# Performance work log

Measured on AMD Instinct MI355X. Metric: run time of the kernel, lower is better.

The kernel has to match this reference:

```python
import jax, jax.numpy as jnp
import numpy as np

N_NODES = 50000


def gcn_conv(x, W, b, row, col, n):
    # PyG GCNConv with default improved=False, add_self_loops=True:
    # h = X W; deg_i = 1 + sum_{e: col==i} 1; out_i = sum_e dinv[row]*dinv[col]*h[row] + h_i/deg_i + b
    h = x @ W  # [N, out]
    ones = jnp.ones(row.shape[0], dtype=x.dtype)
    deg = jax.ops.segment_sum(ones, col, num_segments=n) + 1.0  # self-loop included
    dinv = jax.lax.rsqrt(deg)
    coef = (dinv[row] * dinv[col])[:, None]  # [E,1]
    msg = h[row] * coef  # edge-wise gather (memory bound)
    agg = jax.ops.segment_sum(msg, col, num_segments=n)
    agg = agg + h * (1.0 / deg)[:, None]  # self-loop contribution
    return agg + b


def setup_inputs() -> dict:
    key = jax.random.key(0)
    ks = jax.random.split(key, 7)
    nfeats, nhids, proj = 128, 128, 4
    h2 = nhids + proj  # 132
    x = jax.random.normal(ks[0], (N_NODES, nfeats), dtype=jnp.float32)
    edge_index = jax.random.randint(ks[1], (2, 800000), 0, N_NODES, dtype=jnp.int64)
    s = 1.0 / np.sqrt(nfeats)
    W_proj = jax.random.normal(ks[2], (nfeats, proj), dtype=jnp.float32) * s
    W1 = jax.random.normal(ks[3], (nfeats, nhids), dtype=jnp.float32) * s
    b1 = jax.random.normal(ks[4], (nhids,), dtype=jnp.float32) * 0.01
    s2 = 1.0 / np.sqrt(h2)
    W2 = jax.random.normal(ks[5], (h2, h2), dtype=jnp.float32) * s2
    b2 = jax.random.normal(ks[6], (h2,), dtype=jnp.float32) * 0.01
    return {"edge_index": edge_index, "x": x, "W_proj": W_proj,
            "W1": W1, "b1": b1, "W2": W2, "b2": b2}


def reference(edge_index, x, W_proj, W1, b1, W2, b2):
    row, col = edge_index[0], edge_index[1]
    n = x.shape[0]
    x_proj = x @ W_proj  # [N, proj]
    h = jax.nn.relu(gcn_conv(x, W1, b1, row, col, n))
    # dropout in eval mode (identity)
    h = jnp.concatenate([h, x_proj], axis=1)  # concat skip -> [N, nhids+proj]
    h = gcn_conv(h, W2, b2, row, col, n)
    return jnp.concatenate([h, x_proj], axis=1)  # [N, nhids+2*proj]
```

## Files before the change

kernel.cpp:

```cpp
#include <hip/hip_runtime.h>

#define NN   50000
#define MPAD 50048

#define NB    196
#define SLOTS 48
#define PT_T  512
#define PT_TILE 4096
#define CAP   5888
#define BT    256

typedef __attribute__((ext_vector_type(8))) short bf16x8;
typedef __attribute__((ext_vector_type(4))) float f32x4;
typedef unsigned int  u32;
typedef unsigned short u16;

__device__ __forceinline__ u16 f2bf(float f) {
    u32 u = __float_as_uint(f);
    return (u16)((u + 0x7fffu + ((u >> 16) & 1u)) >> 16);
}
__device__ __forceinline__ float bflo(u32 u) { return __uint_as_float(u << 16); }
__device__ __forceinline__ float bfhi(u32 u) { return __uint_as_float(u & 0xffff0000u); }
__device__ __forceinline__ u32 pack2(float x, float y) {
    return (u32)f2bf(x) | ((u32)f2bf(y) << 16);
}


__global__ void k_zinit(int* __restrict__ gcnt) {
    int i = threadIdx.x;
    if (i < NB) gcnt[i] = 0;
}

__global__ __launch_bounds__(PT_T) void k_bhist(const int* __restrict__ ecol, int E,
                                                int* __restrict__ gcnt) {
    __shared__ int lh[NB];
    int tid = threadIdx.x;
    for (int i = tid; i < NB; i += PT_T) lh[i] = 0;
    __syncthreads();
    int e0 = blockIdx.x * PT_TILE;
#pragma unroll
    for (int j = 0; j < PT_TILE / PT_T; ++j) {
        int e = e0 + j * PT_T + tid;
        if (e < E) atomicAdd(&lh[ecol[e] >> 8], 1);
    }
    __syncthreads();
    for (int i = tid; i < NB; i += PT_T)
        if (lh[i]) atomicAdd(&gcnt[i], lh[i]);
}

__global__ void k_bscan(const int* __restrict__ gcnt, int* __restrict__ gbase,
                        int* __restrict__ gcursor, int* __restrict__ starts, int E) {
    __shared__ int a[256];
    int tid = threadIdx.x;
    int v = (tid < NB) ? gcnt[tid] : 0;
    a[tid] = v;
    __syncthreads();
    for (int off = 1; off < 256; off <<= 1) {
        int add = (tid >= off) ? a[tid - off] : 0;
        __syncthreads();
        a[tid] += add;
        __syncthreads();
    }
    int exc = a[tid] - v;
    if (tid < NB) { gbase[tid] = exc; gcursor[tid] = exc; }
    if (tid == NB - 1) gbase[NB] = a[tid];
    if (tid == 0) starts[NN] = E;
}

__global__ __launch_bounds__(PT_T) void k_part(const int* __restrict__ erow,
                                               const int* __restrict__ ecol, int E,
                                               int* __restrict__ gcursor,
                                               u32* __restrict__ recs) {
    __shared__ int lcnt[NB];
    __shared__ int bbase[NB];
    __shared__ u32 rbuf[NB * SLOTS];
    int tid = threadIdx.x;
    for (int i = tid; i < NB; i += PT_T) lcnt[i] = 0;
    __syncthreads();
    int e0 = blockIdx.x * PT_TILE;
#pragma unroll
    for (int j = 0; j < PT_TILE / PT_T; ++j) {
        int e = e0 + j * PT_T + tid;
        if (e < E) {
            int c = ecol[e];
            u32 rec = ((u32)(c & 255) << 24) | (u32)erow[e];
            int b = c >> 8;
            int pos = atomicAdd(&lcnt[b], 1);
            if (pos < SLOTS) rbuf[b * SLOTS + pos] = rec;
            else {
                int g = atomicAdd(&gcursor[b], 1);
                if (g >= 0 && g < E) recs[g] = rec;
            }
        }
    }
    __syncthreads();
    if (tid < NB) {
        int n = lcnt[tid]; if (n > SLOTS) n = SLOTS;
        bbase[tid] = n ? atomicAdd(&gcursor[tid], n) : 0;
    }
    __syncthreads();
    int wave = tid >> 6, lane = tid & 63;
    for (int b = wave; b < NB; b += PT_T / 64) {
        int n = lcnt[b]; if (n > SLOTS) n = SLOTS;
        if (lane < n) {
            int g = bbase[b] + lane;
            if (g >= 0 && g < E) recs[g] = rbuf[b * SLOTS + lane];
        }
    }
}

__global__ __launch_bounds__(BT) void k_build(const u32* __restrict__ recs,
                                              const int* __restrict__ gbase,
                                              int* __restrict__ starts,
                                              float* __restrict__ dinv,
                                              u32* __restrict__ ec) {
    __shared__ u32 rbuf[CAP];
    __shared__ u32 obuf[CAP];
    __shared__ int ncnt[256];
    __shared__ int a[256];
    __shared__ int ncur[256];
    int tid = threadIdx.x, b = blockIdx.x;
    int lo = gbase[b], hi = gbase[b + 1];
    int cnt = hi - lo;
    bool stage = (cnt > 0) && (cnt <= CAP);
    if (stage) for (int i = tid; i < cnt; i += BT) rbuf[i] = recs[lo + i];
    ncnt[tid] = 0;
    __syncthreads();
    for (int i = tid; i < cnt; i += BT) {
        u32 rec = stage ? rbuf[i] : recs[lo + i];
        atomicAdd(&ncnt[rec >> 24], 1);
    }
    __syncthreads();
    a[tid] = ncnt[tid];
    __syncthreads();
    for (int off = 1; off < 256; off <<= 1) {
        int add = (tid >= off) ? a[tid - off] : 0;
        __syncthreads();
        a[tid] += add;
        __syncthreads();
    }
    int excl = a[tid] - ncnt[tid];
    ncur[tid] = excl;
    {
        int node = (b << 8) + tid;
        if (node < NN) {
            starts[node] = lo + excl;
            float d = (float)ncnt[tid] + 1.0f;
            dinv[node] = rsqrtf(d);
        }
    }
    __syncthreads();
    for (int i = tid; i < cnt; i += BT) {
        u32 rec = stage ? rbuf[i] : recs[lo + i];
        int nl = rec >> 24;
        int pos = atomicAdd(&ncur[nl], 1);
        u32 r = rec & 0xFFFFFFu;
        if (stage) { if (pos >= 0 && pos < CAP) obuf[pos] = r; }
        else if (pos >= 0 && lo + pos < hi) ec[lo + pos] = r;
    }
    __syncthreads();
    if (stage) for (int i = tid; i < cnt; i += BT) ec[lo + i] = obuf[i];
}


__global__ void k_prep_w1(const float* __restrict__ W1, const float* __restrict__ Wp,
                          u16* __restrict__ Wt) {
    int i = blockIdx.x * blockDim.x + threadIdx.x;
    if (i >= 144 * 128) return;
    int n = i >> 7, k = i & 127;
    float v = 0.f;
    if (n < 128) v = W1[k * 128 + n];
    else if (n < 132) v = Wp[k * 4 + (n - 128)];
    Wt[i] = f2bf(v);
}

__global__ void k_prep_w2(const float* __restrict__ W2, u16* __restrict__ Wt) {
    int i = blockIdx.x * blockDim.x + threadIdx.x;
    if (i >= 144 * 160) return;
    int n = i / 160, k = i - n * 160;
    float v = (n < 132 && k < 132) ? W2[k * 132 + n] : 0.f;
    Wt[i] = f2bf(v);
}

template<int K, bool CONVF32, bool SCALE_EXT>
__global__ __launch_bounds__(256) void k_gemm_mfma(const void* __restrict__ Ain,
                                                   const u16* __restrict__ Bt,
                                                   const float* __restrict__ rs,
                                                   u16* __restrict__ Cmain,
                                                   u16* __restrict__ Cext) {
    int lane = threadIdx.x & 63;
    int wv = threadIdx.x >> 6;
    int rbase = blockIdx.x * 64 + wv * 16;
    int lr = lane & 15;
    int kk = (lane >> 4) * 8;
    int arow = rbase + lr;
    if (CONVF32 && arow >= NN) arow = NN - 1;

    const u16* bp = Bt + (size_t)lr * K + kk;

    f32x4 acc[9] = {};
#pragma unroll
    for (int ks = 0; ks < K / 32; ++ks) {
        bf16x8 af;
        if (CONVF32) {
            const float* ap = (const float*)Ain + (size_t)arow * K + kk + ks * 32;
            float4 f0 = *(const float4*)ap;
            float4 f1 = *(const float4*)(ap + 4);
            union { uint4 u; bf16x8 v; } cv;
            cv.u.x = pack2(f0.x, f0.y); cv.u.y = pack2(f0.z, f0.w);
            cv.u.z = pack2(f1.x, f1.y); cv.u.w = pack2(f1.z, f1.w);
            af = cv.v;
        } else {
            af = *(const bf16x8*)((const u16*)Ain + (size_t)arow * K + kk + ks * 32);
        }
#pragma unroll
        for (int t = 0; t < 9; ++t) {
            bf16x8 bf = *(const bf16x8*)(bp + (size_t)(t * 16) * K + ks * 32);
            acc[t] = __builtin_amdgcn_mfma_f32_16x16x32_bf16(bf, af, acc[t], 0, 0, 0);
        }
    }

    int n0 = (lane >> 4) * 4;
    int crow = rbase + lr;
    int srow = crow < NN ? crow : NN - 1;
    float s = rs[srow];
    u16* cm = Cmain + (size_t)crow * 128;
#pragma unroll
    for (int t = 0; t < 8; ++t) {
        ushort4 w;
        w.x = f2bf(acc[t][0] * s); w.y = f2bf(acc[t][1] * s);
        w.z = f2bf(acc[t][2] * s); w.w = f2bf(acc[t][3] * s);
        *(ushort4*)(cm + 16 * t + n0) = w;
    }
    if (n0 == 0) {
        float se = SCALE_EXT ? s : 1.0f;
        ushort4 w;
        w.x = f2bf(acc[8][0] * se); w.y = f2bf(acc[8][1] * se);
        w.z = f2bf(acc[8][2] * se); w.w = f2bf(acc[8][3] * se);
        *(ushort4*)(Cext + (size_t)crow * 4) = w;
    }
}


__global__ void k_agg1(const u16* __restrict__ Hm, const u16* __restrict__ Xp,
                       const int* __restrict__ starts, const u32* __restrict__ ec,
                       const float* __restrict__ dinv,
                       const float* __restrict__ b1, u16* __restrict__ outp) {
    int node = blockIdx.x * (blockDim.x >> 6) + (threadIdx.x >> 6);
    int lane = threadIdx.x & 63;
    if (node >= NN) return;
    int s = starts[node], e = starts[node + 1];

    u32 us = *(const u32*)(Hm + ((size_t)node << 7) + 2 * lane);
    float ax = bflo(us), ay = bfhi(us);
    int i = s;
    for (; i + 8 <= e; i += 8) {
        uint4 qa = *(const uint4*)(ec + i);
        uint4 qb = *(const uint4*)(ec + i + 4);
        u32 u0 = *(const u32*)(Hm + ((size_t)qa.x << 7) + 2 * lane);
        u32 u1 = *(const u32*)(Hm + ((size_t)qa.y << 7) + 2 * lane);
        u32 u2 = *(const u32*)(Hm + ((size_t)qa.z << 7) + 2 * lane);
        u32 u3 = *(const u32*)(Hm + ((size_t)qa.w << 7) + 2 * lane);
        u32 u4 = *(const u32*)(Hm + ((size_t)qb.x << 7) + 2 * lane);
        u32 u5 = *(const u32*)(Hm + ((size_t)qb.y << 7) + 2 * lane);
        u32 u6 = *(const u32*)(Hm + ((size_t)qb.z << 7) + 2 * lane);
        u32 u7 = *(const u32*)(Hm + ((size_t)qb.w << 7) + 2 * lane);
        ax += bflo(u0); ay += bfhi(u0); ax += bflo(u1); ay += bfhi(u1);
        ax += bflo(u2); ay += bfhi(u2); ax += bflo(u3); ay += bfhi(u3);
        ax += bflo(u4); ay += bfhi(u4); ax += bflo(u5); ay += bfhi(u5);
        ax += bflo(u6); ay += bfhi(u6); ax += bflo(u7); ay += bfhi(u7);
    }
    for (; i + 4 <= e; i += 4) {
        uint4 q = *(const uint4*)(ec + i);
        u32 u0 = *(const u32*)(Hm + ((size_t)q.x << 7) + 2 * lane);
        u32 u1 = *(const u32*)(Hm + ((size_t)q.y << 7) + 2 * lane);
        u32 u2 = *(const u32*)(Hm + ((size_t)q.z << 7) + 2 * lane);
        u32 u3 = *(const u32*)(Hm + ((size_t)q.w << 7) + 2 * lane);
        ax += bflo(u0); ay += bfhi(u0); ax += bflo(u1); ay += bfhi(u1);
        ax += bflo(u2); ay += bfhi(u2); ax += bflo(u3); ay += bfhi(u3);
    }
    for (; i < e; ++i) {
        u32 q = ec[i];
        u32 u = *(const u32*)(Hm + ((size_t)q << 7) + 2 * lane);
        ax += bflo(u); ay += bfhi(u);
    }

    float dc = dinv[node];
    float2 bv = *(const float2*)(b1 + 2 * lane);
    float vx = fmaxf(fmaf(dc, ax, bv.x), 0.f);
    float vy = fmaxf(fmaf(dc, ay, bv.y), 0.f);

    u32* orow = (u32*)(outp + (size_t)node * 160);
    orow[lane] = pack2(vx, vy);
    if (lane < 2) orow[64 + lane] = *(const u32*)(Xp + (size_t)node * 4 + 2 * lane);
    else if (lane < 16) orow[64 + lane] = 0;
}

__global__ void k_agg2(const u16* __restrict__ Hm, const u16* __restrict__ He,
                       const u16* __restrict__ Xp1,
                       const int* __restrict__ starts, const u32* __restrict__ ec,
                       const float* __restrict__ dinv,
                       const float* __restrict__ b2, float* __restrict__ outp) {
    int node = blockIdx.x * (blockDim.x >> 6) + (threadIdx.x >> 6);
    int lane = threadIdx.x & 63;
    if (node >= NN) return;
    int s = starts[node], e = starts[node + 1];

    u32 us = *(const u32*)(Hm + ((size_t)node << 7) + 2 * lane);
    float ax = bflo(us), ay = bfhi(us);
    float cx = 0.f, cy = 0.f;
    if (lane < 2) {
        u32 us2 = *(const u32*)(He + ((size_t)node << 2) + 2 * lane);
        cx = bflo(us2); cy = bfhi(us2);
    }
    int i = s;
    for (; i + 8 <= e; i += 8) {
        uint4 qa = *(const uint4*)(ec + i);
        uint4 qb = *(const uint4*)(ec + i + 4);
        u32 u0 = *(const u32*)(Hm + ((size_t)qa.x << 7) + 2 * lane);
        u32 u1 = *(const u32*)(Hm + ((size_t)qa.y << 7) + 2 * lane);
        u32 u2 = *(const u32*)(Hm + ((size_t)qa.z << 7) + 2 * lane);
        u32 u3 = *(const u32*)(Hm + ((size_t)qa.w << 7) + 2 * lane);
        u32 u4 = *(const u32*)(Hm + ((size_t)qb.x << 7) + 2 * lane);
        u32 u5 = *(const u32*)(Hm + ((size_t)qb.y << 7) + 2 * lane);
        u32 u6 = *(const u32*)(Hm + ((size_t)qb.z << 7) + 2 * lane);
        u32 u7 = *(const u32*)(Hm + ((size_t)qb.w << 7) + 2 * lane);
        ax += bflo(u0); ay += bfhi(u0); ax += bflo(u1); ay += bfhi(u1);
        ax += bflo(u2); ay += bfhi(u2); ax += bflo(u3); ay += bfhi(u3);
        ax += bflo(u4); ay += bfhi(u4); ax += bflo(u5); ay += bfhi(u5);
        ax += bflo(u6); ay += bfhi(u6); ax += bflo(u7); ay += bfhi(u7);
        if (lane < 2) {
            u32 e0 = *(const u32*)(He + ((size_t)qa.x << 2) + 2 * lane);
            u32 e1 = *(const u32*)(He + ((size_t)qa.y << 2) + 2 * lane);
            u32 e2 = *(const u32*)(He + ((size_t)qa.z << 2) + 2 * lane);
            u32 e3 = *(const u32*)(He + ((size_t)qa.w << 2) + 2 * lane);
            u32 e4 = *(const u32*)(He + ((size_t)qb.x << 2) + 2 * lane);
            u32 e5 = *(const u32*)(He + ((size_t)qb.y << 2) + 2 * lane);
            u32 e6 = *(const u32*)(He + ((size_t)qb.z << 2) + 2 * lane);
            u32 e7 = *(const u32*)(He + ((size_t)qb.w << 2) + 2 * lane);
            cx += bflo(e0); cy += bfhi(e0); cx += bflo(e1); cy += bfhi(e1);
            cx += bflo(e2); cy += bfhi(e2); cx += bflo(e3); cy += bfhi(e3);
            cx += bflo(e4); cy += bfhi(e4); cx += bflo(e5); cy += bfhi(e5);
            cx += bflo(e6); cy += bfhi(e6); cx += bflo(e7); cy += bfhi(e7);
        }
    }
    for (; i < e; ++i) {
        u32 q = ec[i];
        u32 u = *(const u32*)(Hm + ((size_t)q << 7) + 2 * lane);
        ax += bflo(u); ay += bfhi(u);
        if (lane < 2) {
            u32 e0 = *(const u32*)(He + ((size_t)q << 2) + 2 * lane);
            cx += bflo(e0); cy += bfhi(e0);
        }
    }

    float dc = dinv[node];
    float2 bv = *(const float2*)(b2 + 2 * lane);
    float vx = fmaf(dc, ax, bv.x);
    float vy = fmaf(dc, ay, bv.y);
    float* orow = outp + (size_t)node * 136;
    *(float2*)(orow + 2 * lane) = make_float2(vx, vy);

    if (lane < 2) {
        float2 bb = *(const float2*)(b2 + 128 + 2 * lane);
        float wx = fmaf(dc, cx, bb.x);
        float wy = fmaf(dc, cy, bb.y);
        *(float2*)(orow + 128 + 2 * lane) = make_float2(wx, wy);
        u32 up = *(const u32*)(Xp1 + ((size_t)node << 2) + 2 * lane);
        *(float2*)(orow + 132 + 2 * lane) = make_float2(bflo(up), bfhi(up));
    }
}

extern "C" void kernel_launch(void* const* d_in, const int* in_sizes, int n_in,
                              void* d_out, int out_size, void* d_ws, size_t ws_size,
                              hipStream_t stream) {
    const int*   ei = (const int*)d_in[0];
    const float* x  = (const float*)d_in[1];
    const float* Wp = (const float*)d_in[2];
    const float* W1 = (const float*)d_in[3];
    const float* b1 = (const float*)d_in[4];
    const float* W2 = (const float*)d_in[5];
    const float* b2 = (const float*)d_in[6];
    float* out = (float*)d_out;

    const int E = in_sizes[0] / 2;
    const int* erow = ei;
    const int* ecol = ei + E;

    char* p = (char*)d_ws;
    u16* H1main = (u16*)p; p += (size_t)MPAD * 128 * 2;
    u16* Hcat   = (u16*)p; p += (size_t)MPAD * 160 * 2;
    u16* Xp1    = (u16*)p; p += (size_t)MPAD * 4 * 2;
    u16* H2ext  = (u16*)p; p += (size_t)MPAD * 4 * 2;
    u16* W1t    = (u16*)p; p += 144 * 128 * 2;
    u16* W2t    = (u16*)p; p += 144 * 160 * 2;
    u32* recs   = (u32*)p; p += (size_t)E * 4;
    u32* ec     = (u32*)p; p += (size_t)E * 4;
    float* dinv   = (float*)p; p += NN * 4;
    int* starts = (int*)p; p += (size_t)(NN + 1) * 4;
    int* gcnt   = (int*)p; p += NB * 4;
    int* gbase  = (int*)p; p += (NB + 1) * 4;
    int* gcursor= (int*)p; p += NB * 4;

    u16* H2main = H1main;

    const int T = 256;
    const int pblocks = (E + PT_TILE - 1) / PT_TILE;

    k_prep_w1<<<(144 * 128 + T - 1) / T, T, 0, stream>>>(W1, Wp, W1t);
    k_prep_w2<<<(144 * 160 + T - 1) / T, T, 0, stream>>>(W2, W2t);

    k_zinit<<<1, 256, 0, stream>>>(gcnt);
    k_bhist<<<pblocks, PT_T, 0, stream>>>(ecol, E, gcnt);
    k_bscan<<<1, 256, 0, stream>>>(gcnt, gbase, gcursor, starts, E);
    k_part<<<pblocks, PT_T, 0, stream>>>(erow, ecol, E, gcursor, recs);
    k_build<<<NB, BT, 0, stream>>>(recs, gbase, starts, dinv, ec);

    const int gblocks = MPAD / 64;
    const int ablocks = (NN + 3) / 4;

    k_gemm_mfma<128, true, false><<<gblocks, T, 0, stream>>>(x, W1t, dinv, H1main, Xp1);
    k_agg1<<<ablocks, T, 0, stream>>>(H1main, Xp1, starts, ec, dinv, b1, Hcat);

    k_gemm_mfma<160, false, true><<<gblocks, T, 0, stream>>>(Hcat, W2t, dinv, H2main, H2ext);
    k_agg2<<<ablocks, T, 0, stream>>>(H2main, H2ext, Xp1, starts, ec, dinv, b2, out);
}
```

Before: 173.7 us.

## Split each wave into four 16-lane edge groups with 16-byte gathers

```diff
diff --git a/kernel.cpp b/kernel.cpp
--- a/kernel.cpp
+++ b/kernel.cpp
@@ -2,6 +2,7 @@
 
 #define NN   50000
 #define MPAD 50048
+#define ZR   NN
 
 #define NB    196
 #define SLOTS 48
@@ -222,8 +223,7 @@
 
     int n0 = (lane >> 4) * 4;
     int crow = rbase + lr;
-    int srow = crow < NN ? crow : NN - 1;
-    float s = rs[srow];
+    float s = (crow < NN) ? rs[crow] : 0.0f;
     u16* cm = Cmain + (size_t)crow * 128;
 #pragma unroll
     for (int t = 0; t < 8; ++t) {
@@ -233,7 +233,7 @@
         *(ushort4*)(cm + 16 * t + n0) = w;
     }
     if (n0 == 0) {
-        float se = SCALE_EXT ? s : 1.0f;
+        float se = SCALE_EXT ? s : ((crow < NN) ? 1.0f : 0.0f);
         ushort4 w;
         w.x = f2bf(acc[8][0] * se); w.y = f2bf(acc[8][1] * se);
         w.z = f2bf(acc[8][2] * se); w.w = f2bf(acc[8][3] * se);
@@ -242,61 +242,85 @@
 }
 
 
-__global__ void k_agg1(const u16* __restrict__ Hm, const u16* __restrict__ Xp,
+__global__ __launch_bounds__(256) void k_agg1(const u16* __restrict__ Hm,
+                       const u16* __restrict__ Xp,
                        const int* __restrict__ starts, const u32* __restrict__ ec,
                        const float* __restrict__ dinv,
                        const float* __restrict__ b1, u16* __restrict__ outp) {
     int node = blockIdx.x * (blockDim.x >> 6) + (threadIdx.x >> 6);
     int lane = threadIdx.x & 63;
-    if (node >= NN) return;
+    if (node >= MPAD) return;
+    int c16 = lane & 15;
+    u32* orow = (u32*)(outp + (size_t)node * 160);
+    if (node >= NN) {
+        if (lane < 16) {
+            *(uint4*)(orow + c16 * 4) = make_uint4(0, 0, 0, 0);
+            orow[64 + lane] = 0;
+        }
+        return;
+    }
+    int q = lane >> 4;
     int s = starts[node], e = starts[node + 1];
 
-    u32 us = *(const u32*)(Hm + ((size_t)node << 7) + 2 * lane);
-    float ax = bflo(us), ay = bfhi(us);
-    int i = s;
-    for (; i + 8 <= e; i += 8) {
-        uint4 qa = *(const uint4*)(ec + i);
-        uint4 qb = *(const uint4*)(ec + i + 4);
-        u32 u0 = *(const u32*)(Hm + ((size_t)qa.x << 7) + 2 * lane);
-        u32 u1 = *(const u32*)(Hm + ((size_t)qa.y << 7) + 2 * lane);
-        u32 u2 = *(const u32*)(Hm + ((size_t)qa.z << 7) + 2 * lane);
-        u32 u3 = *(const u32*)(Hm + ((size_t)qa.w << 7) + 2 * lane);
-        u32 u4 = *(const u32*)(Hm + ((size_t)qb.x << 7) + 2 * lane);
-        u32 u5 = *(const u32*)(Hm + ((size_t)qb.y << 7) + 2 * lane);
-        u32 u6 = *(const u32*)(Hm + ((size_t)qb.z << 7) + 2 * lane);
-        u32 u7 = *(const u32*)(Hm + ((size_t)qb.w << 7) + 2 * lane);
-        ax += bflo(u0); ay += bfhi(u0); ax += bflo(u1); ay += bfhi(u1);
-        ax += bflo(u2); ay += bfhi(u2); ax += bflo(u3); ay += bfhi(u3);
-        ax += bflo(u4); ay += bfhi(u4); ax += bflo(u5); ay += bfhi(u5);
-        ax += bflo(u6); ay += bfhi(u6); ax += bflo(u7); ay += bfhi(u7);
-    }
-    for (; i + 4 <= e; i += 4) {
-        uint4 q = *(const uint4*)(ec + i);
-        u32 u0 = *(const u32*)(Hm + ((size_t)q.x << 7) + 2 * lane);
-        u32 u1 = *(const u32*)(Hm + ((size_t)q.y << 7) + 2 * lane);
-        u32 u2 = *(const u32*)(Hm + ((size_t)q.z << 7) + 2 * lane);
-        u32 u3 = *(const u32*)(Hm + ((size_t)q.w << 7) + 2 * lane);
-        ax += bflo(u0); ay += bfhi(u0); ax += bflo(u1); ay += bfhi(u1);
-        ax += bflo(u2); ay += bfhi(u2); ax += bflo(u3); ay += bfhi(u3);
-    }
-    for (; i < e; ++i) {
-        u32 q = ec[i];
-        u32 u = *(const u32*)(Hm + ((size_t)q << 7) + 2 * lane);
-        ax += bflo(u); ay += bfhi(u);
-    }
+    float a0=0,a1=0,a2=0,a3=0,a4=0,a5=0,a6=0,a7=0;
+    if (lane < 16) {
+        uint4 v = *(const uint4*)(Hm + ((size_t)node << 7) + c16 * 8);
+        a0 = bflo(v.x); a1 = bfhi(v.x); a2 = bflo(v.y); a3 = bfhi(v.y);
+        a4 = bflo(v.z); a5 = bfhi(v.z); a6 = bflo(v.w); a7 = bfhi(v.w);
+    }
+
+    for (int g0 = s; g0 < e; g0 += 16) {
+        u32 row[4];
+#pragma unroll
+        for (int grp = 0; grp < 4; ++grp) {
+            int idx = g0 + grp * 4 + q;
+            int ii = idx < e ? idx : e - 1;
+            u32 r = ec[ii];
+            row[grp] = (idx < e) ? r : (u32)ZR;
+        }
+        uint4 v[4];
+#pragma unroll
+        for (int grp = 0; grp < 4; ++grp)
+            v[grp] = *(const uint4*)(Hm + ((size_t)row[grp] << 7) + c16 * 8);
+#pragma unroll
+        for (int grp = 0; grp < 4; ++grp) {
+            a0 += bflo(v[grp].x); a1 += bfhi(v[grp].x);
+            a2 += bflo(v[grp].y); a3 += bfhi(v[grp].y);
+            a4 += bflo(v[grp].z); a5 += bfhi(v[grp].z);
+            a6 += bflo(v[grp].w); a7 += bfhi(v[grp].w);
+        }
+    }
+
+    a0 += __shfl_xor(a0, 16); a1 += __shfl_xor(a1, 16);
+    a2 += __shfl_xor(a2, 16); a3 += __shfl_xor(a3, 16);
+    a4 += __shfl_xor(a4, 16); a5 += __shfl_xor(a5, 16);
+    a6 += __shfl_xor(a6, 16); a7 += __shfl_xor(a7, 16);
+    a0 += __shfl_xor(a0, 32); a1 += __shfl_xor(a1, 32);
+    a2 += __shfl_xor(a2, 32); a3 += __shfl_xor(a3, 32);
+    a4 += __shfl_xor(a4, 32); a5 += __shfl_xor(a5, 32);
+    a6 += __shfl_xor(a6, 32); a7 += __shfl_xor(a7, 32);
 
     float dc = dinv[node];
-    float2 bv = *(const float2*)(b1 + 2 * lane);
-    float vx = fmaxf(fmaf(dc, ax, bv.x), 0.f);
-    float vy = fmaxf(fmaf(dc, ay, bv.y), 0.f);
-
-    u32* orow = (u32*)(outp + (size_t)node * 160);
-    orow[lane] = pack2(vx, vy);
-    if (lane < 2) orow[64 + lane] = *(const u32*)(Xp + (size_t)node * 4 + 2 * lane);
-    else if (lane < 16) orow[64 + lane] = 0;
-}
-
-__global__ void k_agg2(const u16* __restrict__ Hm, const u16* __restrict__ He,
+    float4 bA = *(const float4*)(b1 + c16 * 8);
+    float4 bB = *(const float4*)(b1 + c16 * 8 + 4);
+    float v0 = fmaxf(fmaf(dc, a0, bA.x), 0.f);
+    float v1 = fmaxf(fmaf(dc, a1, bA.y), 0.f);
+    float v2 = fmaxf(fmaf(dc, a2, bA.z), 0.f);
+    float v3 = fmaxf(fmaf(dc, a3, bA.w), 0.f);
+    float v4 = fmaxf(fmaf(dc, a4, bB.x), 0.f);
+    float v5 = fmaxf(fmaf(dc, a5, bB.y), 0.f);
+    float v6 = fmaxf(fmaf(dc, a6, bB.z), 0.f);
+    float v7 = fmaxf(fmaf(dc, a7, bB.w), 0.f);
+
+    if (lane < 16) {
+        uint4 w = make_uint4(pack2(v0, v1), pack2(v2, v3), pack2(v4, v5), pack2(v6, v7));
+        *(uint4*)(orow + c16 * 4) = w;
+        orow[64 + lane] = (lane < 2) ? *(const u32*)(Xp + ((size_t)node << 2) + 2 * lane) : 0u;
+    }
+}
+
+__global__ __launch_bounds__(256) void k_agg2(const u16* __restrict__ Hm,
+                       const u16* __restrict__ He,
                        const u16* __restrict__ Xp1,
                        const int* __restrict__ starts, const u32* __restrict__ ec,
                        const float* __restrict__ dinv,
@@ -304,68 +328,78 @@
     int node = blockIdx.x * (blockDim.x >> 6) + (threadIdx.x >> 6);
     int lane = threadIdx.x & 63;
     if (node >= NN) return;
+    int c16 = lane & 15;
+    int q = lane >> 4;
     int s = starts[node], e = starts[node + 1];
 
-    u32 us = *(const u32*)(Hm + ((size_t)node << 7) + 2 * lane);
-    float ax = bflo(us), ay = bfhi(us);
+    float a0=0,a1=0,a2=0,a3=0,a4=0,a5=0,a6=0,a7=0;
     float cx = 0.f, cy = 0.f;
+    if (lane < 16) {
+        uint4 v = *(const uint4*)(Hm + ((size_t)node << 7) + c16 * 8);
+        a0 = bflo(v.x); a1 = bfhi(v.x); a2 = bflo(v.y); a3 = bfhi(v.y);
+        a4 = bflo(v.z); a5 = bfhi(v.z); a6 = bflo(v.w); a7 = bfhi(v.w);
+    }
     if (lane < 2) {
-        u32 us2 = *(const u32*)(He + ((size_t)node << 2) + 2 * lane);
-        cx = bflo(us2); cy = bfhi(us2);
-    }
-    int i = s;
-    for (; i + 8 <= e; i += 8) {
-        uint4 qa = *(const uint4*)(ec + i);
-        uint4 qb = *(const uint4*)(ec + i + 4);
-        u32 u0 = *(const u32*)(Hm + ((size_t)qa.x << 7) + 2 * lane);
-        u32 u1 = *(const u32*)(Hm + ((size_t)qa.y << 7) + 2 * lane);
-        u32 u2 = *(const u32*)(Hm + ((size_t)qa.z << 7) + 2 * lane);
-        u32 u3 = *(const u32*)(Hm + ((size_t)qa.w << 7) + 2 * lane);
-        u32 u4 = *(const u32*)(Hm + ((size_t)qb.x << 7) + 2 * lane);
-        u32 u5 = *(const u32*)(Hm + ((size_t)qb.y << 7) + 2 * lane);
-        u32 u6 = *(const u32*)(Hm + ((size_t)qb.z << 7) + 2 * lane);
-        u32 u7 = *(const u32*)(Hm + ((size_t)qb.w << 7) + 2 * lane);
-        ax += bflo(u0); ay += bfhi(u0); ax += bflo(u1); ay += bfhi(u1);
-        ax += bflo(u2); ay += bfhi(u2); ax += bflo(u3); ay += bfhi(u3);
-        ax += bflo(u4); ay += bfhi(u4); ax += bflo(u5); ay += bfhi(u5);
-        ax += bflo(u6); ay += bfhi(u6); ax += bflo(u7); ay += bfhi(u7);
-        if (lane < 2) {
-            u32 e0 = *(const u32*)(He + ((size_t)qa.x << 2) + 2 * lane);
-            u32 e1 = *(const u32*)(He + ((size_t)qa.y << 2) + 2 * lane);
-            u32 e2 = *(const u32*)(He + ((size_t)qa.z << 2) + 2 * lane);
-            u32 e3 = *(const u32*)(He + ((size_t)qa.w << 2) + 2 * lane);
-            u32 e4 = *(const u32*)(He + ((size_t)qb.x << 2) + 2 * lane);
-            u32 e5 = *(const u32*)(He + ((size_t)qb.y << 2) + 2 * lane);
-            u32 e6 = *(const u32*)(He + ((size_t)qb.z << 2) + 2 * lane);
-            u32 e7 = *(const u32*)(He + ((size_t)qb.w << 2) + 2 * lane);
-            cx += bflo(e0); cy += bfhi(e0); cx += bflo(e1); cy += bfhi(e1);
-            cx += bflo(e2); cy += bfhi(e2); cx += bflo(e3); cy += bfhi(e3);
-            cx += bflo(e4); cy += bfhi(e4); cx += bflo(e5); cy += bfhi(e5);
-            cx += bflo(e6); cy += bfhi(e6); cx += bflo(e7); cy += bfhi(e7);
-        }
-    }
-    for (; i < e; ++i) {
-        u32 q = ec[i];
-        u32 u = *(const u32*)(Hm + ((size_t)q << 7) + 2 * lane);
-        ax += bflo(u); ay += bfhi(u);
-        if (lane < 2) {
-            u32 e0 = *(const u32*)(He + ((size_t)q << 2) + 2 * lane);
-            cx += bflo(e0); cy += bfhi(e0);
-        }
-    }
+        u32 w = *(const u32*)(He + ((size_t)node << 2) + 2 * lane);
+        cx = bflo(w); cy = bfhi(w);
+    }
+
+    for (int g0 = s; g0 < e; g0 += 16) {
+        u32 row[4];
+#pragma unroll
+        for (int grp = 0; grp < 4; ++grp) {
+            int idx = g0 + grp * 4 + q;
+            int ii = idx < e ? idx : e - 1;
+            u32 r = ec[ii];
+            row[grp] = (idx < e) ? r : (u32)ZR;
+        }
+        uint4 v[4];
+#pragma unroll
+        for (int grp = 0; grp < 4; ++grp)
+            v[grp] = *(const uint4*)(Hm + ((size_t)row[grp] << 7) + c16 * 8);
+        if (c16 < 2) {
+#pragma unroll
+            for (int grp = 0; grp < 4; ++grp) {
+                u32 w = *(const u32*)(He + ((size_t)row[grp] << 2) + 2 * (lane & 1));
+                cx += bflo(w); cy += bfhi(w);
+            }
+        }
+#pragma unroll
+        for (int grp = 0; grp < 4; ++grp) {
+            a0 += bflo(v[grp].x); a1 += bfhi(v[grp].x);
+            a2 += bflo(v[grp].y); a3 += bfhi(v[grp].y);
+            a4 += bflo(v[grp].z); a5 += bfhi(v[grp].z);
+            a6 += bflo(v[grp].w); a7 += bfhi(v[grp].w);
+        }
+    }
+
+    a0 += __shfl_xor(a0, 16); a1 += __shfl_xor(a1, 16);
+    a2 += __shfl_xor(a2, 16); a3 += __shfl_xor(a3, 16);
+    a4 += __shfl_xor(a4, 16); a5 += __shfl_xor(a5, 16);
+    a6 += __shfl_xor(a6, 16); a7 += __shfl_xor(a7, 16);
+    cx += __shfl_xor(cx, 16); cy += __shfl_xor(cy, 16);
+    a0 += __shfl_xor(a0, 32); a1 += __shfl_xor(a1, 32);
+    a2 += __shfl_xor(a2, 32); a3 += __shfl_xor(a3, 32);
+    a4 += __shfl_xor(a4, 32); a5 += __shfl_xor(a5, 32);
+    a6 += __shfl_xor(a6, 32); a7 += __shfl_xor(a7, 32);
+    cx += __shfl_xor(cx, 32); cy += __shfl_xor(cy, 32);
 
     float dc = dinv[node];
-    float2 bv = *(const float2*)(b2 + 2 * lane);
-    float vx = fmaf(dc, ax, bv.x);
-    float vy = fmaf(dc, ay, bv.y);
     float* orow = outp + (size_t)node * 136;
-    *(float2*)(orow + 2 * lane) = make_float2(vx, vy);
-
+    if (lane < 16) {
+        float4 bA = *(const float4*)(b2 + c16 * 8);
+        float4 bB = *(const float4*)(b2 + c16 * 8 + 4);
+        float4 wA, wB;
+        wA.x = fmaf(dc, a0, bA.x); wA.y = fmaf(dc, a1, bA.y);
+        wA.z = fmaf(dc, a2, bA.z); wA.w = fmaf(dc, a3, bA.w);
+        wB.x = fmaf(dc, a4, bB.x); wB.y = fmaf(dc, a5, bB.y);
+        wB.z = fmaf(dc, a6, bB.z); wB.w = fmaf(dc, a7, bB.w);
+        *(float4*)(orow + c16 * 8) = wA;
+        *(float4*)(orow + c16 * 8 + 4) = wB;
+    }
     if (lane < 2) {
         float2 bb = *(const float2*)(b2 + 128 + 2 * lane);
-        float wx = fmaf(dc, cx, bb.x);
-        float wy = fmaf(dc, cy, bb.y);
-        *(float2*)(orow + 128 + 2 * lane) = make_float2(wx, wy);
+        *(float2*)(orow + 128 + 2 * lane) = make_float2(fmaf(dc, cx, bb.x), fmaf(dc, cy, bb.y));
         u32 up = *(const u32*)(Xp1 + ((size_t)node << 2) + 2 * lane);
         *(float2*)(orow + 132 + 2 * lane) = make_float2(bflo(up), bfhi(up));
     }
@@ -396,7 +430,7 @@
     u16* W2t    = (u16*)p; p += 144 * 160 * 2;
     u32* recs   = (u32*)p; p += (size_t)E * 4;
     u32* ec     = (u32*)p; p += (size_t)E * 4;
-    float* dinv   = (float*)p; p += NN * 4;
+    float* dinv = (float*)p; p += NN * 4;
     int* starts = (int*)p; p += (size_t)(NN + 1) * 4;
     int* gcnt   = (int*)p; p += NB * 4;
     int* gbase  = (int*)p; p += (NB + 1) * 4;
@@ -417,11 +451,12 @@
     k_build<<<NB, BT, 0, stream>>>(recs, gbase, starts, dinv, ec);
 
     const int gblocks = MPAD / 64;
-    const int ablocks = (NN + 3) / 4;
+    const int a1blocks = (MPAD + 3) / 4;
+    const int a2blocks = (NN + 3) / 4;
 
     k_gemm_mfma<128, true, false><<<gblocks, T, 0, stream>>>(x, W1t, dinv, H1main, Xp1);
-    k_agg1<<<ablocks, T, 0, stream>>>(H1main, Xp1, starts, ec, dinv, b1, Hcat);
+    k_agg1<<<a1blocks, T, 0, stream>>>(H1main, Xp1, starts, ec, dinv, b1, Hcat);
 
     k_gemm_mfma<160, false, true><<<gblocks, T, 0, stream>>>(Hcat, W2t, dinv, H2main, H2ext);
-    k_agg2<<<ablocks, T, 0, stream>>>(H2main, H2ext, Xp1, starts, ec, dinv, b2, out);
-}
+    k_agg2<<<a2blocks, T, 0, stream>>>(H2main, H2ext, Xp1, starts, ec, dinv, b2, out);
+}
```

Result: faster. 159.9 us (-7.9%).
